# Kernel tuning notes

Hardware: AMD Instinct MI355X
Metric: run time of the kernel (lower is better)

Reference implementation:

```python
import jax, jax.numpy as jnp
import numpy as np

WIN = 9
PAD = WIN // 2
ALPHA = 0.1
BETA = 0.1
EPS_NCC = 1e-5
EPS_SC = 1e-5


def box_sum(x):
    """All-ones WIN^3 box-filter local sum, stride 1, pad WIN//2.
    Implemented separably (3 1-D convs) -- mathematically identical to the
    original single F.conv3d with a ones [1,1,9,9,9] kernel, far cheaper.
    x: [N, 1, D, H, W]"""
    for axis in range(3):
        kshape = [1, 1, 1, 1, 1]
        kshape[2 + axis] = WIN
        kern = jnp.ones(kshape, x.dtype)
        pad = [(0, 0), (0, 0), (0, 0)]
        pad[axis] = (PAD, PAD)
        x = jax.lax.conv_general_dilated(x, kern, (1, 1, 1), pad)
    return x


def setup_inputs() -> dict:
    key = jax.random.key(0)
    k1, k2, k3, k4, k5 = jax.random.split(key, 5)
    B, T, D, H, W = 1, 4, 128, 128, 128
    image = jax.random.normal(k1, (B, T, D, H, W), jnp.float32)
    mask = jax.random.uniform(k2, (B, T, D, H, W), jnp.float32)
    pred_image = jax.random.normal(k3, (B, T, D, H, W), jnp.float32)
    pred_mask = jax.random.uniform(k4, (B, T, D, H, W), jnp.float32)
    flow = jax.random.normal(k5, (T - 1, B, 3, D, H, W), jnp.float32)
    time_diff = jnp.arange(B * T, dtype=jnp.float32).reshape(B, T)
    return {"image": image, "mask": mask, "pred_image": pred_image,
            "pred_mask": pred_mask, "flow": flow, "time_diff": time_diff}


def reference(image, mask, pred_image, pred_mask, flow, time_diff):
    B, T, D, H, W = image.shape
    win_size = WIN ** 3

    # ---- NCC loss: fixed frame (t=0) vs each predicted frame t=1..T-1 ----
    # Per-t (1 - mean(cc_t)) averaged over T-1 equals 1 - mean over the
    # stacked batch since every cc_t has identical shape.
    I = jnp.broadcast_to(image[:, :1], (B, T - 1, D, H, W)).reshape(B * (T - 1), 1, D, H, W)
    J = pred_image[:, 1:].reshape(B * (T - 1), 1, D, H, W)
    I_sum = box_sum(I)
    J_sum = box_sum(J)
    I2_sum = box_sum(I * I)
    J2_sum = box_sum(J * J)
    IJ_sum = box_sum(I * J)
    u_I = I_sum / win_size
    u_J = J_sum / win_size
    cross = IJ_sum - u_J * I_sum - u_I * J_sum + u_I * u_J * win_size
    I_var = I2_sum - 2 * u_I * I_sum + u_I * u_I * win_size
    J_var = J2_sum - 2 * u_J * J_sum + u_J * u_J * win_size
    cc = cross * cross / (I_var * J_var + EPS_NCC)
    ncc = 1.0 - jnp.mean(cc)

    # ---- gradient (flow smoothness) loss, l2 penalty ----
    # flow: [T-1, B, 3, D, H, W]; per-t means of equal-shaped diffs average
    # to the global mean over the leading t axis.
    dy = jnp.square(jnp.abs(flow[:, :, :, 1:, :, :] - flow[:, :, :, :-1, :, :]))
    dx = jnp.square(jnp.abs(flow[:, :, :, :, 1:, :] - flow[:, :, :, :, :-1, :]))
    dz = jnp.square(jnp.abs(flow[:, :, :, :, :, 1:] - flow[:, :, :, :, :, :-1]))
    grad_loss = (jnp.mean(dx) + jnp.mean(dy) + jnp.mean(dz)) / 3.0

    # ---- temporal volume smoothness constraint ----
    area = jnp.sum(pred_mask, axis=(2, 3, 4)).T  # [T, B]
    area = area / jnp.max(area)
    scs = []
    for i in range(T - 2):
        for j in range(i + 1, T - 1):
            for k in range(j + 1, T):
                lam = (time_diff[:, j] - time_diff[:, i] + EPS_SC) / (
                    time_diff[:, k] - time_diff[:, i] + EPS_SC)
                scs.append(jnp.square(area[j] - area[i] - lam * (area[k] - area[i])))
    sc = jnp.mean(jnp.stack(scs, axis=1))

    return ncc + ALPHA * grad_loss + BETA * sc
```

## Files before the change

kernel.cpp:

```cpp
#include <hip/hip_runtime.h>

#define V3 (128 * 128 * 128)

typedef _Float16 h8 __attribute__((ext_vector_type(8)));
typedef float    f8 __attribute__((ext_vector_type(8)));

__device__ __forceinline__ float block_reduce(float v, float* sm) {
#pragma unroll
  for (int off = 32; off > 0; off >>= 1) v += __shfl_down(v, off, 64);
  int lane = threadIdx.x & 63;
  int wid  = threadIdx.x >> 6;
  if (lane == 0) sm[wid] = v;
  __syncthreads();
  float r = 0.f;
  if ((int)threadIdx.x < (int)(blockDim.x >> 6)) r = sm[threadIdx.x];
  if (wid == 0) {
#pragma unroll
    for (int off = 4; off > 0; off >>= 1) r += __shfl_down(r, off, 64);
  }
  __syncthreads();
  return r;
}

__device__ __forceinline__ f8 ldh(const _Float16* __restrict__ p, size_t off,
                                  float m) {
  h8 q = *(const h8*)(p + off);
  f8 r = __builtin_convertvector(q, f8);
  return r * m;
}

__global__ __launch_bounds__(256) void area_kernel(const float* __restrict__ pm,
                                                   float* __restrict__ acc) {
  __shared__ float sm[8];
  const int t = blockIdx.y;
  const float* p = pm + (size_t)t * V3;
  const int n4 = V3 / 4;
  float s = 0.f;
  for (int i = blockIdx.x * blockDim.x + threadIdx.x; i < n4;
       i += gridDim.x * blockDim.x) {
    float4 a = *(const float4*)(p + 4 * (size_t)i);
    s += (a.x + a.y) + (a.z + a.w);
  }
  s = block_reduce(s, sm);
  if (threadIdx.x == 0) atomicAdd(acc + t, s);
}

__global__ __launch_bounds__(256) void grad_kernel(const float* __restrict__ fl,
                                                   float* __restrict__ acc) {
  __shared__ float sm[8];
  const int w4 = threadIdx.x & 31;
  const int hl = threadIdx.x >> 5;
  const int h  = blockIdx.x * 8 + hl;
  const int d0 = blockIdx.y * 16;
  const int c  = blockIdx.z;
  const float* p = fl + (size_t)c * V3 + (size_t)h * 128 + w4 * 4;
  const bool hv = (h < 127);

  float s = 0.f;
  float4 cur  = *(const float4*)(p + (size_t)d0 * 16384);
  float4 curh = hv ? *(const float4*)(p + (size_t)d0 * 16384 + 128) : cur;

#pragma unroll
  for (int dd = 0; dd < 16; ++dd) {
    const int d = d0 + dd;
    const bool dv = (d < 127);
    float4 nxt = cur, nxth = curh;
    if (dv) {
      nxt = *(const float4*)(p + (size_t)(d + 1) * 16384);
      if (hv) nxth = *(const float4*)(p + (size_t)(d + 1) * 16384 + 128);
    }
    float x;
    x = cur.y - cur.x; s += x * x;
    x = cur.z - cur.y; s += x * x;
    x = cur.w - cur.z; s += x * x;
    float nx = __shfl_down(cur.x, 1, 64);
    if (w4 != 31) { x = nx - cur.w; s += x * x; }
    if (hv) {
      x = curh.x - cur.x; s += x * x;
      x = curh.y - cur.y; s += x * x;
      x = curh.z - cur.z; s += x * x;
      x = curh.w - cur.w; s += x * x;
    }
    if (dv) {
      x = nxt.x - cur.x; s += x * x;
      x = nxt.y - cur.y; s += x * x;
      x = nxt.z - cur.z; s += x * x;
      x = nxt.w - cur.w; s += x * x;
    }
    cur = nxt; curh = nxth;
  }
  s = block_reduce(s, sm);
  if (threadIdx.x == 0) atomicAdd(acc, s);
}

template <bool WITH_I>
__global__ __launch_bounds__(256) void n1_kernel(const float* __restrict__ I0,
                                                 const float* __restrict__ Jall,
                                                 _Float16* __restrict__ FI,
                                                 _Float16* __restrict__ FJall) {
  constexpr int NF = WITH_I ? 5 : 3;
  __shared__ float sI[2][2][136];
  __shared__ float sJ[2][2][136];
  __shared__ float ring[2][9][NF][128];

  const int tz = blockIdx.z;
  const float* J = Jall + (size_t)tz * V3;
  _Float16* FJ = FJall + (size_t)tz * 3 * (size_t)V3;

  const int w  = threadIdx.x & 127;
  const int dl = threadIdx.x >> 7;
  const int d  = blockIdx.y * 2 + dl;
  const int h0 = blockIdx.x * 16;
  const float* Ib = I0 + (size_t)d * 16384;
  const float* Jb = J  + (size_t)d * 16384;

  if (w < 4) {
    sI[dl][0][w] = 0.f; sI[dl][1][w] = 0.f;
    sJ[dl][0][w] = 0.f; sJ[dl][1][w] = 0.f;
  }
  if (w >= 124) {
    sI[dl][0][w + 8] = 0.f; sI[dl][1][w + 8] = 0.f;
    sJ[dl][0][w + 8] = 0.f; sJ[dl][1][w + 8] = 0.f;
  }
#pragma unroll
  for (int sl = 0; sl < 9; ++sl)
#pragma unroll
    for (int f = 0; f < NF; ++f) ring[dl][sl][f][w] = 0.f;

  auto stage = [&](int hh) {
    if (hh >= 0 && hh < 128) {
      const int b = hh & 1;
      if (w < 32) {
        float4 v = *(const float4*)(Ib + hh * 128 + w * 4);
        *(float4*)&sI[dl][b][4 + w * 4] = v;
      } else if (w < 64) {
        const int l = w - 32;
        float4 v = *(const float4*)(Jb + hh * 128 + l * 4);
        *(float4*)&sJ[dl][b][4 + l * 4] = v;
      }
    }
  };

  float S[NF];
#pragma unroll
  for (int f = 0; f < NF; ++f) S[f] = 0.f;

  stage(h0 - 4);
  int slot = (h0 + 32) % 9;

  for (int hh = h0 - 4; hh < h0 + 20; ++hh) {
    __syncthreads();
    stage(hh + 1);
    const int b = hh & 1;
    const bool valid = (hh >= 0) && (hh < 128);

    float Wn[NF];
#pragma unroll
    for (int f = 0; f < NF; ++f) Wn[f] = 0.f;
    if (valid) {
#pragma unroll
      for (int k = 0; k < 9; ++k) {
        float a = sI[dl][b][w + k];
        float bb = sJ[dl][b][w + k];
        if (WITH_I) {
          Wn[0] += a; Wn[1] += a * a;
          Wn[2] += bb; Wn[3] += bb * bb; Wn[4] += a * bb;
        } else {
          Wn[0] += bb; Wn[1] += bb * bb; Wn[2] += a * bb;
        }
      }
    }

#pragma unroll
    for (int f = 0; f < NF; ++f) {
      float old = ring[dl][slot][f][w];
      ring[dl][slot][f][w] = Wn[f];
      S[f] += Wn[f] - old;
    }
    ++slot; if (slot == 9) slot = 0;

    const int ho = hh - 4;
    if (ho >= h0) {
      size_t base = (size_t)d * 16384 + (size_t)ho * 128 + w;
      if (WITH_I) {
        FI[base]                  = (_Float16)S[0];
        FI[(size_t)V3 + base]     = (_Float16)S[1];
        FJ[base]                  = (_Float16)S[2];
        FJ[(size_t)V3 + base]     = (_Float16)S[3];
        FJ[2 * (size_t)V3 + base] = (_Float16)S[4];
      } else {
        FJ[base]                  = (_Float16)S[0];
        FJ[(size_t)V3 + base]     = (_Float16)S[1];
        FJ[2 * (size_t)V3 + base] = (_Float16)S[2];
      }
    }
  }
}

__global__ __launch_bounds__(128) void n2_kernel(const _Float16* __restrict__ FI,
                                                 const _Float16* __restrict__ FJall,
                                                 float* __restrict__ acc) {
  __shared__ float sm[8];
  const _Float16* FJ = FJall + (size_t)blockIdx.z * 3 * (size_t)V3;
  const int w8 = threadIdx.x & 15;
  const int h  = blockIdx.x * 8 + (threadIdx.x >> 4);
  const int d0 = blockIdx.y * 8;
  const size_t hw = (size_t)h * 128 + w8 * 8;

  const _Float16* P0 = FI;
  const _Float16* P1 = FI + (size_t)V3;
  const _Float16* P2 = FJ;
  const _Float16* P3 = FJ + (size_t)V3;
  const _Float16* P4 = FJ + 2 * (size_t)V3;

  f8 S0 = {}, S1 = {}, S2 = {}, S3 = {}, S4 = {};
#pragma unroll
  for (int k = 0; k < 9; ++k) {
    const int dd = d0 - 4 + k;
    const float m = (dd >= 0) ? 1.f : 0.f;
    const size_t a = (size_t)(dd >= 0 ? dd : 0) * 16384 + hw;
    S0 += ldh(P0, a, m);
    S1 += ldh(P1, a, m);
    S2 += ldh(P2, a, m);
    S3 += ldh(P3, a, m);
    S4 += ldh(P4, a, m);
  }

  const float inv_win = 1.0f / 729.0f;
  float accv = 0.f;
#pragma unroll
  for (int dd = 0; dd < 8; ++dd) {
    const int d = d0 + dd;
    f8 cross = S4 - S0 * S2 * inv_win;
    f8 iv    = S1 - S0 * S0 * inv_win;
    f8 jv    = S3 - S2 * S2 * inv_win;
    f8 den   = iv * jv + 1e-5f;
#pragma unroll
    for (int i = 0; i < 8; ++i)
      accv += cross[i] * cross[i] * __builtin_amdgcn_rcpf(den[i]);

    const int da = d + 5, ds = d - 4;
    const float ma = (da < 128) ? 1.f : 0.f;
    const float ms = (ds >= 0) ? 1.f : 0.f;
    const size_t aa = (size_t)(da < 128 ? da : 0) * 16384 + hw;
    const size_t as = (size_t)(ds >= 0 ? ds : 0) * 16384 + hw;
    S0 += ldh(P0, aa, ma) - ldh(P0, as, ms);
    S1 += ldh(P1, aa, ma) - ldh(P1, as, ms);
    S2 += ldh(P2, aa, ma) - ldh(P2, as, ms);
    S3 += ldh(P3, aa, ma) - ldh(P3, as, ms);
    S4 += ldh(P4, aa, ma) - ldh(P4, as, ms);
  }

  accv = block_reduce(accv, sm);
  if (threadIdx.x == 0) atomicAdd(acc, accv);
}

__global__ void final_kernel(const float* __restrict__ ws,
                             const float* __restrict__ td,
                             float* __restrict__ out) {
  if (threadIdx.x != 0 || blockIdx.x != 0) return;
  float area[4];
  float amax = -1e30f;
#pragma unroll
  for (int t = 0; t < 4; ++t) {
    area[t] = ws[t];
    amax = fmaxf(amax, area[t]);
  }
  float a[4];
#pragma unroll
  for (int t = 0; t < 4; ++t) a[t] = area[t] / amax;

  float sc = 0.f;
  int cnt = 0;
  for (int i = 0; i < 2; ++i)
    for (int j = i + 1; j < 3; ++j)
      for (int k = j + 1; k < 4; ++k) {
        float lam = (td[j] - td[i] + 1e-5f) / (td[k] - td[i] + 1e-5f);
        float e = a[j] - a[i] - lam * (a[k] - a[i]);
        sc += e * e;
        ++cnt;
      }
  sc /= (float)cnt;

  float ncc  = 1.0f - ws[7] / (3.0f * (float)V3);
  float grad = ws[4] / (3.0f * 9.0f * 127.0f * 128.0f * 128.0f);
  out[0] = ncc + 0.1f * grad + 0.1f * sc;
}

extern "C" void kernel_launch(void* const* d_in, const int* in_sizes, int n_in,
                              void* d_out, int out_size, void* d_ws, size_t ws_size,
                              hipStream_t stream) {
  const float* image      = (const float*)d_in[0];
  const float* pred_image = (const float*)d_in[2];
  const float* pred_mask  = (const float*)d_in[3];
  const float* flow       = (const float*)d_in[4];
  const float* time_diff  = (const float*)d_in[5];
  float* out = (float*)d_out;
  float* wsf = (float*)d_ws;
  _Float16* FI = (_Float16*)(wsf + 64);
  _Float16* FJ = FI + 2 * (size_t)V3;

  hipMemsetAsync(d_ws, 0, 256, stream);

  hipLaunchKernelGGL(area_kernel, dim3(512, 4), dim3(256), 0, stream,
                     pred_mask, wsf);
  hipLaunchKernelGGL(grad_kernel, dim3(16, 8, 9), dim3(256), 0, stream,
                     flow, wsf + 4);

  const size_t need_fused = 256 + 11 * (size_t)V3 * sizeof(_Float16);
  if (ws_size >= need_fused) {
    hipLaunchKernelGGL((n1_kernel<true>), dim3(8, 64, 1), dim3(256), 0, stream,
                       image, pred_image + (size_t)V3, FI, FJ);
    hipLaunchKernelGGL((n1_kernel<false>), dim3(8, 64, 2), dim3(256), 0, stream,
                       image, pred_image + 2 * (size_t)V3, FI,
                       FJ + 3 * (size_t)V3);
    hipLaunchKernelGGL(n2_kernel, dim3(16, 16, 3), dim3(128), 0, stream,
                       FI, FJ, wsf + 7);
  } else {
    for (int t = 0; t < 3; ++t) {
      const float* J = pred_image + (size_t)(t + 1) * V3;
      if (t == 0) {
        hipLaunchKernelGGL((n1_kernel<true>), dim3(8, 64, 1), dim3(256), 0,
                           stream, image, J, FI, FJ);
      } else {
        hipLaunchKernelGGL((n1_kernel<false>), dim3(8, 64, 1), dim3(256), 0,
                           stream, image, J, FI, FJ);
      }
      hipLaunchKernelGGL(n2_kernel, dim3(16, 16, 1), dim3(128), 0, stream,
                         FI, FJ, wsf + 7);
    }
  }

  hipLaunchKernelGGL(final_kernel, dim3(1), dim3(1), 0, stream,
                     wsf, time_diff, out);
}
```

Before: 132.5 us.

## Move n1 ring buffer to registers, merge n1 launches, halve n2 depth tile

The 9-slot running-sum ring for the H-axis box filter moves from shared memory into a register array shifted each step, and the template split is removed so all three frames run in one n1 launch that always computes five sums (writing the FI planes only for t=0). n2 now processes 4 depth slices per block instead of 8, doubling the grid, and gains an upper-bound guard on its preload. This aims to drop shared-memory ring traffic, cut one launch, and raise n2 parallelism. The costs are higher register pressure from the 45-float ring and its shift moves, redundant I-sum arithmetic for t=1,2, and more redundant 9-slice preloads in n2.

```diff
diff --git a/kernel.cpp b/kernel.cpp
--- a/kernel.cpp
+++ b/kernel.cpp
@@ -93,19 +93,18 @@
   if (threadIdx.x == 0) atomicAdd(acc, s);
 }
 
-template <bool WITH_I>
 __global__ __launch_bounds__(256) void n1_kernel(const float* __restrict__ I0,
-                                                 const float* __restrict__ Jall,
+                                                 const float* __restrict__ Jbase,
                                                  _Float16* __restrict__ FI,
-                                                 _Float16* __restrict__ FJall) {
-  constexpr int NF = WITH_I ? 5 : 3;
+                                                 _Float16* __restrict__ FJbase,
+                                                 int t_of_z0) {
   __shared__ float sI[2][2][136];
   __shared__ float sJ[2][2][136];
-  __shared__ float ring[2][9][NF][128];
-
-  const int tz = blockIdx.z;
-  const float* J = Jall + (size_t)tz * V3;
-  _Float16* FJ = FJall + (size_t)tz * 3 * (size_t)V3;
+
+  const int tz = t_of_z0 + blockIdx.z;
+  const bool with_i = (tz == 0);
+  const float* J = Jbase + (size_t)blockIdx.z * V3;
+  _Float16* FJ = FJbase + (size_t)blockIdx.z * 3 * (size_t)V3;
 
   const int w  = threadIdx.x & 127;
   const int dl = threadIdx.x >> 7;
@@ -122,10 +121,6 @@
     sI[dl][0][w + 8] = 0.f; sI[dl][1][w + 8] = 0.f;
     sJ[dl][0][w + 8] = 0.f; sJ[dl][1][w + 8] = 0.f;
   }
-#pragma unroll
-  for (int sl = 0; sl < 9; ++sl)
-#pragma unroll
-    for (int f = 0; f < NF; ++f) ring[dl][sl][f][w] = 0.f;
 
   auto stage = [&](int hh) {
     if (hh >= 0 && hh < 128) {
@@ -141,12 +136,14 @@
     }
   };
 
-  float S[NF];
-#pragma unroll
-  for (int f = 0; f < NF; ++f) S[f] = 0.f;
+  float ring[9][5];
+#pragma unroll
+  for (int sl = 0; sl < 9; ++sl)
+#pragma unroll
+    for (int f = 0; f < 5; ++f) ring[sl][f] = 0.f;
+  float S[5] = {0.f, 0.f, 0.f, 0.f, 0.f};
 
   stage(h0 - 4);
-  int slot = (h0 + 32) % 9;
 
   for (int hh = h0 - 4; hh < h0 + 20; ++hh) {
     __syncthreads();
@@ -154,45 +151,36 @@
     const int b = hh & 1;
     const bool valid = (hh >= 0) && (hh < 128);
 
-    float Wn[NF];
-#pragma unroll
-    for (int f = 0; f < NF; ++f) Wn[f] = 0.f;
+    float Wn[5] = {0.f, 0.f, 0.f, 0.f, 0.f};
     if (valid) {
 #pragma unroll
       for (int k = 0; k < 9; ++k) {
-        float a = sI[dl][b][w + k];
+        float a  = sI[dl][b][w + k];
         float bb = sJ[dl][b][w + k];
-        if (WITH_I) {
-          Wn[0] += a; Wn[1] += a * a;
-          Wn[2] += bb; Wn[3] += bb * bb; Wn[4] += a * bb;
-        } else {
-          Wn[0] += bb; Wn[1] += bb * bb; Wn[2] += a * bb;
-        }
+        Wn[0] += a;  Wn[1] += a * a;
+        Wn[2] += bb; Wn[3] += bb * bb; Wn[4] += a * bb;
       }
     }
 
 #pragma unroll
-    for (int f = 0; f < NF; ++f) {
-      float old = ring[dl][slot][f][w];
-      ring[dl][slot][f][w] = Wn[f];
-      S[f] += Wn[f] - old;
-    }
-    ++slot; if (slot == 9) slot = 0;
+    for (int f = 0; f < 5; ++f) S[f] += Wn[f] - ring[0][f];
+#pragma unroll
+    for (int sl = 0; sl < 8; ++sl)
+#pragma unroll
+      for (int f = 0; f < 5; ++f) ring[sl][f] = ring[sl + 1][f];
+#pragma unroll
+    for (int f = 0; f < 5; ++f) ring[8][f] = Wn[f];
 
     const int ho = hh - 4;
     if (ho >= h0) {
       size_t base = (size_t)d * 16384 + (size_t)ho * 128 + w;
-      if (WITH_I) {
-        FI[base]                  = (_Float16)S[0];
-        FI[(size_t)V3 + base]     = (_Float16)S[1];
-        FJ[base]                  = (_Float16)S[2];
-        FJ[(size_t)V3 + base]     = (_Float16)S[3];
-        FJ[2 * (size_t)V3 + base] = (_Float16)S[4];
-      } else {
-        FJ[base]                  = (_Float16)S[0];
-        FJ[(size_t)V3 + base]     = (_Float16)S[1];
-        FJ[2 * (size_t)V3 + base] = (_Float16)S[2];
+      if (with_i) {
+        FI[base]              = (_Float16)S[0];
+        FI[(size_t)V3 + base] = (_Float16)S[1];
       }
+      FJ[base]                  = (_Float16)S[2];
+      FJ[(size_t)V3 + base]     = (_Float16)S[3];
+      FJ[2 * (size_t)V3 + base] = (_Float16)S[4];
     }
   }
 }
@@ -204,7 +192,7 @@
   const _Float16* FJ = FJall + (size_t)blockIdx.z * 3 * (size_t)V3;
   const int w8 = threadIdx.x & 15;
   const int h  = blockIdx.x * 8 + (threadIdx.x >> 4);
-  const int d0 = blockIdx.y * 8;
+  const int d0 = blockIdx.y * 4;
   const size_t hw = (size_t)h * 128 + w8 * 8;
 
   const _Float16* P0 = FI;
@@ -217,8 +205,9 @@
 #pragma unroll
   for (int k = 0; k < 9; ++k) {
     const int dd = d0 - 4 + k;
-    const float m = (dd >= 0) ? 1.f : 0.f;
-    const size_t a = (size_t)(dd >= 0 ? dd : 0) * 16384 + hw;
+    const bool v = (dd >= 0) && (dd < 128);
+    const float m = v ? 1.f : 0.f;
+    const size_t a = (size_t)(v ? dd : 0) * 16384 + hw;
     S0 += ldh(P0, a, m);
     S1 += ldh(P1, a, m);
     S2 += ldh(P2, a, m);
@@ -229,7 +218,7 @@
   const float inv_win = 1.0f / 729.0f;
   float accv = 0.f;
 #pragma unroll
-  for (int dd = 0; dd < 8; ++dd) {
+  for (int dd = 0; dd < 4; ++dd) {
     const int d = d0 + dd;
     f8 cross = S4 - S0 * S2 * inv_win;
     f8 iv    = S1 - S0 * S0 * inv_win;
@@ -309,24 +298,15 @@
 
   const size_t need_fused = 256 + 11 * (size_t)V3 * sizeof(_Float16);
   if (ws_size >= need_fused) {
-    hipLaunchKernelGGL((n1_kernel<true>), dim3(8, 64, 1), dim3(256), 0, stream,
-                       image, pred_image + (size_t)V3, FI, FJ);
-    hipLaunchKernelGGL((n1_kernel<false>), dim3(8, 64, 2), dim3(256), 0, stream,
-                       image, pred_image + 2 * (size_t)V3, FI,
-                       FJ + 3 * (size_t)V3);
-    hipLaunchKernelGGL(n2_kernel, dim3(16, 16, 3), dim3(128), 0, stream,
+    hipLaunchKernelGGL(n1_kernel, dim3(8, 64, 3), dim3(256), 0, stream,
+                       image, pred_image + (size_t)V3, FI, FJ, 0);
+    hipLaunchKernelGGL(n2_kernel, dim3(16, 32, 3), dim3(128), 0, stream,
                        FI, FJ, wsf + 7);
   } else {
     for (int t = 0; t < 3; ++t) {
-      const float* J = pred_image + (size_t)(t + 1) * V3;
-      if (t == 0) {
-        hipLaunchKernelGGL((n1_kernel<true>), dim3(8, 64, 1), dim3(256), 0,
-                           stream, image, J, FI, FJ);
-      } else {
-        hipLaunchKernelGGL((n1_kernel<false>), dim3(8, 64, 1), dim3(256), 0,
-                           stream, image, J, FI, FJ);
-      }
-      hipLaunchKernelGGL(n2_kernel, dim3(16, 16, 1), dim3(128), 0, stream,
+      hipLaunchKernelGGL(n1_kernel, dim3(8, 64, 1), dim3(256), 0, stream,
+                         image, pred_image + (size_t)(t + 1) * V3, FI, FJ, t);
+      hipLaunchKernelGGL(n2_kernel, dim3(16, 32, 1), dim3(128), 0, stream,
                          FI, FJ, wsf + 7);
     }
   }
```

After: 153.9 us. +16.2%, slower.

## Lengthen n1 H-tiles, store ring in fp16, shrink n2 blocks to one wave

Applied to the files above, without the earlier changes.

n1 now processes 32 output rows per block instead of 16, which halves the redundant 8-row halo work per block. The sliding-window ring buffer moves to fp16 shared memory and is primed with an unrolled 9-step prologue, so the zero-init pass disappears. Each window contribution is rounded to fp16 before it enters the running sum so adds and subtracts cancel exactly. n2 is split into 64-thread single-wave blocks (twice as many, half as wide in W) and uses only a shuffle reduction, dropping shared memory and syncs; the trade is fewer blocks for n1 and extra fp16 rounding in the sums.

```diff
diff --git a/kernel.cpp b/kernel.cpp
--- a/kernel.cpp
+++ b/kernel.cpp
@@ -95,22 +95,21 @@
 
 template <bool WITH_I>
 __global__ __launch_bounds__(256) void n1_kernel(const float* __restrict__ I0,
-                                                 const float* __restrict__ Jall,
+                                                 const float* __restrict__ Jbase,
                                                  _Float16* __restrict__ FI,
-                                                 _Float16* __restrict__ FJall) {
+                                                 _Float16* __restrict__ FJbase) {
   constexpr int NF = WITH_I ? 5 : 3;
   __shared__ float sI[2][2][136];
   __shared__ float sJ[2][2][136];
-  __shared__ float ring[2][9][NF][128];
-
-  const int tz = blockIdx.z;
-  const float* J = Jall + (size_t)tz * V3;
-  _Float16* FJ = FJall + (size_t)tz * 3 * (size_t)V3;
+  __shared__ _Float16 ring[2][9][NF][128];
+
+  const float* J = Jbase + (size_t)blockIdx.z * V3;
+  _Float16* FJ = FJbase + (size_t)blockIdx.z * 3 * (size_t)V3;
 
   const int w  = threadIdx.x & 127;
   const int dl = threadIdx.x >> 7;
   const int d  = blockIdx.y * 2 + dl;
-  const int h0 = blockIdx.x * 16;
+  const int h0 = blockIdx.x * 32;
   const float* Ib = I0 + (size_t)d * 16384;
   const float* Jb = J  + (size_t)d * 16384;
 
@@ -122,10 +121,6 @@
     sI[dl][0][w + 8] = 0.f; sI[dl][1][w + 8] = 0.f;
     sJ[dl][0][w + 8] = 0.f; sJ[dl][1][w + 8] = 0.f;
   }
-#pragma unroll
-  for (int sl = 0; sl < 9; ++sl)
-#pragma unroll
-    for (int f = 0; f < NF; ++f) ring[dl][sl][f][w] = 0.f;
 
   auto stage = [&](int hh) {
     if (hh >= 0 && hh < 128) {
@@ -141,70 +136,88 @@
     }
   };
 
-  float S[NF];
-#pragma unroll
-  for (int f = 0; f < NF; ++f) S[f] = 0.f;
-
-  stage(h0 - 4);
-  int slot = (h0 + 32) % 9;
-
-  for (int hh = h0 - 4; hh < h0 + 20; ++hh) {
-    __syncthreads();
-    stage(hh + 1);
-    const int b = hh & 1;
-    const bool valid = (hh >= 0) && (hh < 128);
-
-    float Wn[NF];
+  auto taps = [&](int b, bool valid, float* Wn) {
 #pragma unroll
     for (int f = 0; f < NF; ++f) Wn[f] = 0.f;
     if (valid) {
 #pragma unroll
       for (int k = 0; k < 9; ++k) {
-        float a = sI[dl][b][w + k];
+        float a  = sI[dl][b][w + k];
         float bb = sJ[dl][b][w + k];
         if (WITH_I) {
-          Wn[0] += a; Wn[1] += a * a;
+          Wn[0] += a;  Wn[1] += a * a;
           Wn[2] += bb; Wn[3] += bb * bb; Wn[4] += a * bb;
         } else {
           Wn[0] += bb; Wn[1] += bb * bb; Wn[2] += a * bb;
         }
       }
     }
-
+  };
+
+  auto writeout = [&](int ho, const float* S) {
+    size_t base = (size_t)d * 16384 + (size_t)ho * 128 + w;
+    if (WITH_I) {
+      FI[base]                  = (_Float16)S[0];
+      FI[(size_t)V3 + base]     = (_Float16)S[1];
+      FJ[base]                  = (_Float16)S[2];
+      FJ[(size_t)V3 + base]     = (_Float16)S[3];
+      FJ[2 * (size_t)V3 + base] = (_Float16)S[4];
+    } else {
+      FJ[base]                  = (_Float16)S[0];
+      FJ[(size_t)V3 + base]     = (_Float16)S[1];
+      FJ[2 * (size_t)V3 + base] = (_Float16)S[2];
+    }
+  };
+
+  float S[NF];
+#pragma unroll
+  for (int f = 0; f < NF; ++f) S[f] = 0.f;
+
+  stage(h0 - 4);
+
+#pragma unroll
+  for (int i = 0; i < 9; ++i) {
+    const int hh = h0 - 4 + i;
+    __syncthreads();
+    stage(hh + 1);
+    const int b = hh & 1;
+    float Wn[NF];
+    taps(b, hh >= 0, Wn);
 #pragma unroll
     for (int f = 0; f < NF; ++f) {
-      float old = ring[dl][slot][f][w];
-      ring[dl][slot][f][w] = Wn[f];
-      S[f] += Wn[f] - old;
-    }
-    ++slot; if (slot == 9) slot = 0;
-
-    const int ho = hh - 4;
-    if (ho >= h0) {
-      size_t base = (size_t)d * 16384 + (size_t)ho * 128 + w;
-      if (WITH_I) {
-        FI[base]                  = (_Float16)S[0];
-        FI[(size_t)V3 + base]     = (_Float16)S[1];
-        FJ[base]                  = (_Float16)S[2];
-        FJ[(size_t)V3 + base]     = (_Float16)S[3];
-        FJ[2 * (size_t)V3 + base] = (_Float16)S[4];
-      } else {
-        FJ[base]                  = (_Float16)S[0];
-        FJ[(size_t)V3 + base]     = (_Float16)S[1];
-        FJ[2 * (size_t)V3 + base] = (_Float16)S[2];
-      }
-    }
-  }
-}
-
-__global__ __launch_bounds__(128) void n2_kernel(const _Float16* __restrict__ FI,
-                                                 const _Float16* __restrict__ FJall,
-                                                 float* __restrict__ acc) {
-  __shared__ float sm[8];
+      float wr = (float)(_Float16)Wn[f];
+      ring[dl][i][f][w] = (_Float16)wr;
+      S[f] += wr;
+    }
+  }
+  writeout(h0, S);
+
+  int slot = 0;
+  for (int hh = h0 + 5; hh < h0 + 36; ++hh) {
+    __syncthreads();
+    stage(hh + 1);
+    const int b = hh & 1;
+    float Wn[NF];
+    taps(b, hh < 128, Wn);
+#pragma unroll
+    for (int f = 0; f < NF; ++f) {
+      float wr  = (float)(_Float16)Wn[f];
+      float old = (float)ring[dl][slot][f][w];
+      ring[dl][slot][f][w] = (_Float16)wr;
+      S[f] += wr - old;
+    }
+    slot = (slot == 8) ? 0 : slot + 1;
+    writeout(hh - 4, S);
+  }
+}
+
+__global__ __launch_bounds__(64, 2) void n2_kernel(const _Float16* __restrict__ FI,
+                                                   const _Float16* __restrict__ FJall,
+                                                   float* __restrict__ acc) {
   const _Float16* FJ = FJall + (size_t)blockIdx.z * 3 * (size_t)V3;
-  const int w8 = threadIdx.x & 15;
-  const int h  = blockIdx.x * 8 + (threadIdx.x >> 4);
-  const int d0 = blockIdx.y * 8;
+  const int w8 = (threadIdx.x & 7) + ((blockIdx.y & 1) << 3);
+  const int h  = blockIdx.x * 8 + (threadIdx.x >> 3);
+  const int d0 = (blockIdx.y >> 1) * 8;
   const size_t hw = (size_t)h * 128 + w8 * 8;
 
   const _Float16* P0 = FI;
@@ -217,8 +230,9 @@
 #pragma unroll
   for (int k = 0; k < 9; ++k) {
     const int dd = d0 - 4 + k;
-    const float m = (dd >= 0) ? 1.f : 0.f;
-    const size_t a = (size_t)(dd >= 0 ? dd : 0) * 16384 + hw;
+    const bool v = (dd >= 0) && (dd < 128);
+    const float m = v ? 1.f : 0.f;
+    const size_t a = (size_t)(v ? dd : 0) * 16384 + hw;
     S0 += ldh(P0, a, m);
     S1 += ldh(P1, a, m);
     S2 += ldh(P2, a, m);
@@ -251,7 +265,8 @@
     S4 += ldh(P4, aa, ma) - ldh(P4, as, ms);
   }
 
-  accv = block_reduce(accv, sm);
+#pragma unroll
+  for (int off = 32; off > 0; off >>= 1) accv += __shfl_down(accv, off, 64);
   if (threadIdx.x == 0) atomicAdd(acc, accv);
 }
 
@@ -309,24 +324,24 @@
 
   const size_t need_fused = 256 + 11 * (size_t)V3 * sizeof(_Float16);
   if (ws_size >= need_fused) {
-    hipLaunchKernelGGL((n1_kernel<true>), dim3(8, 64, 1), dim3(256), 0, stream,
+    hipLaunchKernelGGL((n1_kernel<true>), dim3(4, 64, 1), dim3(256), 0, stream,
                        image, pred_image + (size_t)V3, FI, FJ);
-    hipLaunchKernelGGL((n1_kernel<false>), dim3(8, 64, 2), dim3(256), 0, stream,
+    hipLaunchKernelGGL((n1_kernel<false>), dim3(4, 64, 2), dim3(256), 0, stream,
                        image, pred_image + 2 * (size_t)V3, FI,
                        FJ + 3 * (size_t)V3);
-    hipLaunchKernelGGL(n2_kernel, dim3(16, 16, 3), dim3(128), 0, stream,
+    hipLaunchKernelGGL(n2_kernel, dim3(16, 32, 3), dim3(64), 0, stream,
                        FI, FJ, wsf + 7);
   } else {
     for (int t = 0; t < 3; ++t) {
       const float* J = pred_image + (size_t)(t + 1) * V3;
       if (t == 0) {
-        hipLaunchKernelGGL((n1_kernel<true>), dim3(8, 64, 1), dim3(256), 0,
+        hipLaunchKernelGGL((n1_kernel<true>), dim3(4, 64, 1), dim3(256), 0,
                            stream, image, J, FI, FJ);
       } else {
-        hipLaunchKernelGGL((n1_kernel<false>), dim3(8, 64, 1), dim3(256), 0,
+        hipLaunchKernelGGL((n1_kernel<false>), dim3(4, 64, 1), dim3(256), 0,
                            stream, image, J, FI, FJ);
       }
-      hipLaunchKernelGGL(n2_kernel, dim3(16, 16, 1), dim3(128), 0, stream,
+      hipLaunchKernelGGL(n2_kernel, dim3(16, 32, 1), dim3(64), 0, stream,
                          FI, FJ, wsf + 7);
     }
   }
```

Result: slower. 178.4 us (+34.6%).

## Split n2 depth sweep into 2-slice chunks per thread for more parallelism

Applied to the files above, without the earlier changes.

Each n2 thread now computes two depth outputs from ten loaded slices instead of sliding a window across eight outputs, and blocks grow to 256 threads with twice the grid in y. This raises the number of resident waves to hide load latency and shortens the serial dependency chain. In exchange it adds redundant loads of the fp16 box-sum planes, which go up per output.

```diff
diff --git a/kernel.cpp b/kernel.cpp
--- a/kernel.cpp
+++ b/kernel.cpp
@@ -197,14 +197,16 @@
   }
 }
 
-__global__ __launch_bounds__(128) void n2_kernel(const _Float16* __restrict__ FI,
+__global__ __launch_bounds__(256) void n2_kernel(const _Float16* __restrict__ FI,
                                                  const _Float16* __restrict__ FJall,
                                                  float* __restrict__ acc) {
   __shared__ float sm[8];
   const _Float16* FJ = FJall + (size_t)blockIdx.z * 3 * (size_t)V3;
   const int w8 = threadIdx.x & 15;
-  const int h  = blockIdx.x * 8 + (threadIdx.x >> 4);
-  const int d0 = blockIdx.y * 8;
+  const int hl = (threadIdx.x >> 4) & 7;
+  const int dc = threadIdx.x >> 7;
+  const int h  = blockIdx.x * 8 + hl;
+  const int d0 = blockIdx.y * 4 + dc * 2;
   const size_t hw = (size_t)h * 128 + w8 * 8;
 
   const _Float16* P0 = FI;
@@ -214,41 +216,49 @@
   const _Float16* P4 = FJ + 2 * (size_t)V3;
 
   f8 S0 = {}, S1 = {}, S2 = {}, S3 = {}, S4 = {};
-#pragma unroll
-  for (int k = 0; k < 9; ++k) {
+  f8 lo0, lo1, lo2, lo3, lo4, hi0, hi1, hi2, hi3, hi4;
+
+#pragma unroll
+  for (int k = 0; k < 10; ++k) {
     const int dd = d0 - 4 + k;
-    const float m = (dd >= 0) ? 1.f : 0.f;
-    const size_t a = (size_t)(dd >= 0 ? dd : 0) * 16384 + hw;
-    S0 += ldh(P0, a, m);
-    S1 += ldh(P1, a, m);
-    S2 += ldh(P2, a, m);
-    S3 += ldh(P3, a, m);
-    S4 += ldh(P4, a, m);
+    const bool v = (dd >= 0) && (dd < 128);
+    const float m = v ? 1.f : 0.f;
+    const size_t a = (size_t)(v ? dd : 0) * 16384 + hw;
+    f8 q0 = ldh(P0, a, m);
+    f8 q1 = ldh(P1, a, m);
+    f8 q2 = ldh(P2, a, m);
+    f8 q3 = ldh(P3, a, m);
+    f8 q4 = ldh(P4, a, m);
+    if (k == 0) {
+      lo0 = q0; lo1 = q1; lo2 = q2; lo3 = q3; lo4 = q4;
+    } else if (k == 9) {
+      hi0 = q0; hi1 = q1; hi2 = q2; hi3 = q3; hi4 = q4;
+    } else {
+      S0 += q0; S1 += q1; S2 += q2; S3 += q3; S4 += q4;
+    }
   }
 
   const float inv_win = 1.0f / 729.0f;
   float accv = 0.f;
-#pragma unroll
-  for (int dd = 0; dd < 8; ++dd) {
-    const int d = d0 + dd;
-    f8 cross = S4 - S0 * S2 * inv_win;
-    f8 iv    = S1 - S0 * S0 * inv_win;
-    f8 jv    = S3 - S2 * S2 * inv_win;
-    f8 den   = iv * jv + 1e-5f;
+  {
+    f8 A0 = S0 + lo0, A1 = S1 + lo1, A2 = S2 + lo2, A3 = S3 + lo3, A4 = S4 + lo4;
+    f8 cr = A4 - A0 * A2 * inv_win;
+    f8 iv = A1 - A0 * A0 * inv_win;
+    f8 jv = A3 - A2 * A2 * inv_win;
+    f8 den = iv * jv + 1e-5f;
 #pragma unroll
     for (int i = 0; i < 8; ++i)
-      accv += cross[i] * cross[i] * __builtin_amdgcn_rcpf(den[i]);
-
-    const int da = d + 5, ds = d - 4;
-    const float ma = (da < 128) ? 1.f : 0.f;
-    const float ms = (ds >= 0) ? 1.f : 0.f;
-    const size_t aa = (size_t)(da < 128 ? da : 0) * 16384 + hw;
-    const size_t as = (size_t)(ds >= 0 ? ds : 0) * 16384 + hw;
-    S0 += ldh(P0, aa, ma) - ldh(P0, as, ms);
-    S1 += ldh(P1, aa, ma) - ldh(P1, as, ms);
-    S2 += ldh(P2, aa, ma) - ldh(P2, as, ms);
-    S3 += ldh(P3, aa, ma) - ldh(P3, as, ms);
-    S4 += ldh(P4, aa, ma) - ldh(P4, as, ms);
+      accv += cr[i] * cr[i] * __builtin_amdgcn_rcpf(den[i]);
+  }
+  {
+    f8 A0 = S0 + hi0, A1 = S1 + hi1, A2 = S2 + hi2, A3 = S3 + hi3, A4 = S4 + hi4;
+    f8 cr = A4 - A0 * A2 * inv_win;
+    f8 iv = A1 - A0 * A0 * inv_win;
+    f8 jv = A3 - A2 * A2 * inv_win;
+    f8 den = iv * jv + 1e-5f;
+#pragma unroll
+    for (int i = 0; i < 8; ++i)
+      accv += cr[i] * cr[i] * __builtin_amdgcn_rcpf(den[i]);
   }
 
   accv = block_reduce(accv, sm);
@@ -314,7 +324,7 @@
     hipLaunchKernelGGL((n1_kernel<false>), dim3(8, 64, 2), dim3(256), 0, stream,
                        image, pred_image + 2 * (size_t)V3, FI,
                        FJ + 3 * (size_t)V3);
-    hipLaunchKernelGGL(n2_kernel, dim3(16, 16, 3), dim3(128), 0, stream,
+    hipLaunchKernelGGL(n2_kernel, dim3(16, 32, 3), dim3(256), 0, stream,
                        FI, FJ, wsf + 7);
   } else {
     for (int t = 0; t < 3; ++t) {
@@ -326,7 +336,7 @@
         hipLaunchKernelGGL((n1_kernel<false>), dim3(8, 64, 1), dim3(256), 0,
                            stream, image, J, FI, FJ);
       }
-      hipLaunchKernelGGL(n2_kernel, dim3(16, 16, 1), dim3(128), 0, stream,
+      hipLaunchKernelGGL(n2_kernel, dim3(16, 32, 1), dim3(256), 0, stream,
                          FI, FJ, wsf + 7);
     }
   }
```

New measurement: 139.1 us. 1.05x slower.
